# Kernel optimization log

Hardware: AMD Instinct MI355X
Metric: run time of the kernel (lower is better)

Reference implementation:

```python
import jax, jax.numpy as jnp
import numpy as np

N = 16384
E = 262144

def _deg_norm(idx, n):
    deg = jax.ops.segment_sum(jnp.ones((idx.shape[0],), jnp.float32), idx, num_segments=n)
    return jnp.where(deg > 0, deg ** -0.5, 0.0)  # DGL norm='both' with zero-in-degree allowed

def _graph_conv(x, W, b, edge_src, edge_dst, c_src, c_dst):
    # DGL GraphConv(norm='both'): h = D_in^{-1/2} A D_out^{-1/2} (x W) + b
    h = (x * c_src[:, None]) @ W            # [N, out] (mult-first order; linear, so equivalent)
    msg = h[edge_src]                        # gather over edges [E, out]
    agg = jax.ops.segment_sum(msg, edge_dst, num_segments=x.shape[0])
    return agg * c_dst[:, None] + b

def setup_inputs() -> dict:
    key = jax.random.key(0)
    ks = jax.random.split(key, 8)
    return {
        "features": jax.random.normal(ks[0], (N, 256), jnp.float32),
        "W1": jax.random.normal(ks[1], (256, 128), jnp.float32) * 0.05,
        "b1": jnp.zeros((128,), jnp.float32),
        "Wm": jax.random.normal(ks[2], (128, 64), jnp.float32) * 0.05,
        "bm": jnp.zeros((64,), jnp.float32),
        "Ws": jax.random.normal(ks[3], (128, 64), jnp.float32) * 0.05,
        "bs": jnp.zeros((64,), jnp.float32),
        "noise": jax.random.normal(ks[4], (N, 64), jnp.float32),
        "edge_src": jax.random.randint(ks[5], (E,), 0, N, jnp.int32),
        "edge_dst": jax.random.randint(ks[6], (E,), 0, N, jnp.int32),
    }

def reference(features, W1, b1, Wm, bm, Ws, bs, noise, edge_src, edge_dst):
    n = features.shape[0]
    c_src = _deg_norm(edge_src, n)   # out-degree norm
    c_dst = _deg_norm(edge_dst, n)   # in-degree norm
    h = jax.nn.relu(_graph_conv(features, W1, b1, edge_src, edge_dst, c_src, c_dst))
    mean = _graph_conv(h, Wm, bm, edge_src, edge_dst, c_src, c_dst)
    log_std = _graph_conv(h, Ws, bs, edge_src, edge_dst, c_src, c_dst)
    z = mean + noise * jnp.exp(log_std)      # reparameterization
    # InnerProductDecoder with act=identity (dropout inactive at eval), then sigmoid
    pre = jax.nn.sigmoid(z @ z.T)            # [N, N]
    return (pre, z)
```

## Files before the change

kernel.cpp:

```cpp
#include <hip/hip_runtime.h>
#include <hip/hip_bf16.h>


typedef short short8 __attribute__((ext_vector_type(8)));
typedef short short4v __attribute__((ext_vector_type(4)));
typedef float f32x4 __attribute__((ext_vector_type(4)));

__device__ __forceinline__ float bf2f(short s) {
  unsigned int u = ((unsigned int)(unsigned short)s) << 16;
  return __uint_as_float(u);
}

__global__ void k_deg(const int* __restrict__ src, const int* __restrict__ dst,
                      float* __restrict__ cs, float* __restrict__ cd, int E) {
  int i = blockIdx.x * blockDim.x + threadIdx.x;
  if (i < E) {
    atomicAdd(&cs[src[i]], 1.0f);
    atomicAdd(&cd[dst[i]], 1.0f);
  }
}

__global__ void __launch_bounds__(256) k_scan(const float* __restrict__ cnt,
                                              int* __restrict__ off, int n) {
  __shared__ int sums[256];
  const int t = threadIdx.x;
  const int per = n / 256;
  const int base = t * per;
  int s = 0;
  for (int i = 0; i < per; ++i) s += (int)cnt[base + i];
  sums[t] = s;
  __syncthreads();
  for (int d = 1; d < 256; d <<= 1) {
    int v = (t >= d) ? sums[t - d] : 0;
    __syncthreads();
    sums[t] += v;
    __syncthreads();
  }
  int run = t ? sums[t - 1] : 0;
  for (int i = 0; i < per; ++i) { off[base + i] = run; run += (int)cnt[base + i]; }
  if (t == 255) off[n] = run;
}

__global__ void k_cnorm(float* __restrict__ cs, float* __restrict__ cd, int n) {
  int i = blockIdx.x * blockDim.x + threadIdx.x;
  if (i < n) {
    float a = cs[i]; cs[i] = (a > 0.f) ? rsqrtf(a) : 0.f;
    float b = cd[i]; cd[i] = (b > 0.f) ? rsqrtf(b) : 0.f;
  }
}

__global__ void k_fill(const int* __restrict__ src, const int* __restrict__ dst,
                       const int* __restrict__ off, int* __restrict__ cursor,
                       int* __restrict__ elist, int E) {
  int e = blockIdx.x * blockDim.x + threadIdx.x;
  if (e < E) {
    int d = dst[e];
    int pos = atomicAdd(&cursor[d], 1);
    elist[off[d] + pos] = src[e];
  }
}

__global__ void k_wprep1(const float* __restrict__ W, short* __restrict__ hi,
                         short* __restrict__ lo) {
  int idx = blockIdx.x * 256 + threadIdx.x;
  int c = idx >> 8, k = idx & 255;
  float v = W[k * 128 + c];
  __hip_bfloat16 hb = __float2bfloat16(v);
  float hf = __bfloat162float(hb);
  __hip_bfloat16 lb = __float2bfloat16(v - hf);
  hi[c * 256 + k] = *reinterpret_cast<short*>(&hb);
  lo[c * 256 + k] = *reinterpret_cast<short*>(&lb);
}

__global__ void k_wprep2(const float* __restrict__ Wm, const float* __restrict__ Ws,
                         short* __restrict__ hi, short* __restrict__ lo) {
  int idx = blockIdx.x * 256 + threadIdx.x;
  int c = idx >> 7, k = idx & 127;
  float v = (c < 64) ? Wm[k * 64 + c] : Ws[k * 64 + (c - 64)];
  __hip_bfloat16 hb = __float2bfloat16(v);
  float hf = __bfloat162float(hb);
  __hip_bfloat16 lb = __float2bfloat16(v - hf);
  hi[c * 128 + k] = *reinterpret_cast<short*>(&hb);
  lo[c * 128 + k] = *reinterpret_cast<short*>(&lb);
}

__global__ void __launch_bounds__(256) k_enc1(const float* __restrict__ x,
                                              const short* __restrict__ wt_hi,
                                              const short* __restrict__ wt_lo,
                                              const float* __restrict__ cs,
                                              __hip_bfloat16* __restrict__ out) {
  const int wave = threadIdx.x >> 6, lane = threadIdx.x & 63;
  const int lrow = lane & 15, kq = lane >> 4;
  const int brow = blockIdx.x * 64;
  const int bcol = wave * 32;

  f32x4 acc[4][2];
#pragma unroll
  for (int i = 0; i < 4; ++i)
#pragma unroll
    for (int j = 0; j < 2; ++j) acc[i][j] = (f32x4){0.f, 0.f, 0.f, 0.f};

  float crow[4];
#pragma unroll
  for (int i = 0; i < 4; ++i) crow[i] = cs[brow + i * 16 + lrow];

  for (int ks = 0; ks < 8; ++ks) {
    short8 ahi[4], alo[4];
#pragma unroll
    for (int i = 0; i < 4; ++i) {
      const float* ap = x + (size_t)(brow + i * 16 + lrow) * 256 + ks * 32 + kq * 8;
      f32x4 a0 = *reinterpret_cast<const f32x4*>(ap);
      f32x4 a1 = *reinterpret_cast<const f32x4*>(ap + 4);
      const float c = crow[i];
      float vals[8] = {a0.x, a0.y, a0.z, a0.w, a1.x, a1.y, a1.z, a1.w};
      short8 h, l;
#pragma unroll
      for (int j = 0; j < 8; ++j) {
        float v = vals[j] * c;
        __hip_bfloat16 hb = __float2bfloat16(v);
        float hf = __bfloat162float(hb);
        __hip_bfloat16 lb = __float2bfloat16(v - hf);
        h[j] = *reinterpret_cast<short*>(&hb);
        l[j] = *reinterpret_cast<short*>(&lb);
      }
      ahi[i] = h; alo[i] = l;
    }
    short8 bhi[2], blo[2];
#pragma unroll
    for (int j = 0; j < 2; ++j) {
      size_t boff = (size_t)(bcol + j * 16 + lrow) * 256 + ks * 32 + kq * 8;
      bhi[j] = *reinterpret_cast<const short8*>(wt_hi + boff);
      blo[j] = *reinterpret_cast<const short8*>(wt_lo + boff);
    }
#pragma unroll
    for (int i = 0; i < 4; ++i)
#pragma unroll
      for (int j = 0; j < 2; ++j) {
        acc[i][j] = __builtin_amdgcn_mfma_f32_16x16x32_bf16(ahi[i], bhi[j], acc[i][j], 0, 0, 0);
        acc[i][j] = __builtin_amdgcn_mfma_f32_16x16x32_bf16(ahi[i], blo[j], acc[i][j], 0, 0, 0);
        acc[i][j] = __builtin_amdgcn_mfma_f32_16x16x32_bf16(alo[i], bhi[j], acc[i][j], 0, 0, 0);
      }
  }
#pragma unroll
  for (int i = 0; i < 4; ++i)
#pragma unroll
    for (int r = 0; r < 4; ++r) {
      int row = brow + i * 16 + kq * 4 + r;
#pragma unroll
      for (int j = 0; j < 2; ++j)
        out[(size_t)row * 128 + bcol + j * 16 + lrow] = __float2bfloat16(acc[i][j][r]);
    }
}

__global__ void __launch_bounds__(256) k_gather1(const short* __restrict__ tmp,
                                                 const int* __restrict__ off,
                                                 const int* __restrict__ elist,
                                                 const float* __restrict__ cd,
                                                 const float* __restrict__ cs,
                                                 const float* __restrict__ b,
                                                 short* __restrict__ hs) {
  const int node = blockIdx.x * 4 + (threadIdx.x >> 6);
  const int lane = threadIdx.x & 63;
  const int half = lane >> 5;
  const int c4 = (lane & 31) << 2;
  const int e0 = off[node], e1 = off[node + 1];
  f32x4 a = {0.f, 0.f, 0.f, 0.f};
  for (int e = e0 + half; e < e1; e += 2) {
    short4v v = *reinterpret_cast<const short4v*>(tmp + (size_t)elist[e] * 128 + c4);
    a.x += bf2f(v[0]); a.y += bf2f(v[1]); a.z += bf2f(v[2]); a.w += bf2f(v[3]);
  }
  a.x += __shfl_xor(a.x, 32);
  a.y += __shfl_xor(a.y, 32);
  a.z += __shfl_xor(a.z, 32);
  a.w += __shfl_xor(a.w, 32);
  if (half == 0) {
    const float c = cd[node], s = cs[node];
    f32x4 bb = *reinterpret_cast<const f32x4*>(b + c4);
    short4v r;
    {
      __hip_bfloat16 t0 = __float2bfloat16(fmaxf(a.x * c + bb.x, 0.f) * s);
      __hip_bfloat16 t1 = __float2bfloat16(fmaxf(a.y * c + bb.y, 0.f) * s);
      __hip_bfloat16 t2 = __float2bfloat16(fmaxf(a.z * c + bb.z, 0.f) * s);
      __hip_bfloat16 t3 = __float2bfloat16(fmaxf(a.w * c + bb.w, 0.f) * s);
      r[0] = *reinterpret_cast<short*>(&t0);
      r[1] = *reinterpret_cast<short*>(&t1);
      r[2] = *reinterpret_cast<short*>(&t2);
      r[3] = *reinterpret_cast<short*>(&t3);
    }
    *reinterpret_cast<short4v*>(hs + (size_t)node * 128 + c4) = r;
  }
}

__global__ void __launch_bounds__(256) k_gather2(const short* __restrict__ hs,
                                                 const int* __restrict__ off,
                                                 const int* __restrict__ elist,
                                                 const float* __restrict__ cd,
                                                 float* __restrict__ s2c) {
  const int node = blockIdx.x * 4 + (threadIdx.x >> 6);
  const int lane = threadIdx.x & 63;
  const int half = lane >> 5;
  const int c4 = (lane & 31) << 2;
  const int e0 = off[node], e1 = off[node + 1];
  f32x4 a = {0.f, 0.f, 0.f, 0.f};
  for (int e = e0 + half; e < e1; e += 2) {
    short4v v = *reinterpret_cast<const short4v*>(hs + (size_t)elist[e] * 128 + c4);
    a.x += bf2f(v[0]); a.y += bf2f(v[1]); a.z += bf2f(v[2]); a.w += bf2f(v[3]);
  }
  a.x += __shfl_xor(a.x, 32);
  a.y += __shfl_xor(a.y, 32);
  a.z += __shfl_xor(a.z, 32);
  a.w += __shfl_xor(a.w, 32);
  if (half == 0) {
    const float c = cd[node];
    *reinterpret_cast<f32x4*>(s2c + (size_t)node * 128 + c4) = a * c;
  }
}

__global__ void __launch_bounds__(256) k_zfin2(const float* __restrict__ s2c,
                                               const short* __restrict__ wt_hi,
                                               const short* __restrict__ wt_lo,
                                               const float* __restrict__ bm,
                                               const float* __restrict__ bs,
                                               const float* __restrict__ noise,
                                               float* __restrict__ z,
                                               __hip_bfloat16* __restrict__ zb) {
  __shared__ float ys[64][128];
  const int wave = threadIdx.x >> 6, lane = threadIdx.x & 63;
  const int lrow = lane & 15, kq = lane >> 4;
  const int brow = blockIdx.x * 64;
  const int bcol = wave * 32;

  f32x4 acc[4][2];
#pragma unroll
  for (int i = 0; i < 4; ++i)
#pragma unroll
    for (int j = 0; j < 2; ++j) acc[i][j] = (f32x4){0.f, 0.f, 0.f, 0.f};

  for (int ks = 0; ks < 4; ++ks) {
    short8 ahi[4], alo[4];
#pragma unroll
    for (int i = 0; i < 4; ++i) {
      const float* ap = s2c + (size_t)(brow + i * 16 + lrow) * 128 + ks * 32 + kq * 8;
      f32x4 a0 = *reinterpret_cast<const f32x4*>(ap);
      f32x4 a1 = *reinterpret_cast<const f32x4*>(ap + 4);
      float vals[8] = {a0.x, a0.y, a0.z, a0.w, a1.x, a1.y, a1.z, a1.w};
      short8 h, l;
#pragma unroll
      for (int j = 0; j < 8; ++j) {
        float v = vals[j];
        __hip_bfloat16 hb = __float2bfloat16(v);
        float hf = __bfloat162float(hb);
        __hip_bfloat16 lb = __float2bfloat16(v - hf);
        h[j] = *reinterpret_cast<short*>(&hb);
        l[j] = *reinterpret_cast<short*>(&lb);
      }
      ahi[i] = h; alo[i] = l;
    }
    short8 bhi[2], blo[2];
#pragma unroll
    for (int j = 0; j < 2; ++j) {
      size_t boff = (size_t)(bcol + j * 16 + lrow) * 128 + ks * 32 + kq * 8;
      bhi[j] = *reinterpret_cast<const short8*>(wt_hi + boff);
      blo[j] = *reinterpret_cast<const short8*>(wt_lo + boff);
    }
#pragma unroll
    for (int i = 0; i < 4; ++i)
#pragma unroll
      for (int j = 0; j < 2; ++j) {
        acc[i][j] = __builtin_amdgcn_mfma_f32_16x16x32_bf16(ahi[i], bhi[j], acc[i][j], 0, 0, 0);
        acc[i][j] = __builtin_amdgcn_mfma_f32_16x16x32_bf16(ahi[i], blo[j], acc[i][j], 0, 0, 0);
        acc[i][j] = __builtin_amdgcn_mfma_f32_16x16x32_bf16(alo[i], bhi[j], acc[i][j], 0, 0, 0);
      }
  }
#pragma unroll
  for (int j = 0; j < 2; ++j) {
    const int col = bcol + j * 16 + lrow;
    const float bias = (col < 64) ? bm[col] : bs[col - 64];
#pragma unroll
    for (int i = 0; i < 4; ++i)
#pragma unroll
      for (int r = 0; r < 4; ++r)
        ys[i * 16 + kq * 4 + r][col] = acc[i][j][r] + bias;
  }
  __syncthreads();
  const int t = threadIdx.x;
#pragma unroll
  for (int q = 0; q < 16; ++q) {
    int idx = t + 256 * q;
    int row = idx >> 6, c = idx & 63;
    float m = ys[row][c], ls = ys[row][c + 64];
    float zv = m + noise[(size_t)(brow + row) * 64 + c] * __expf(ls);
    z[(size_t)(brow + row) * 64 + c]  = zv;
    zb[(size_t)(brow + row) * 64 + c] = __float2bfloat16(zv);
  }
}

__global__ void __launch_bounds__(256) k_zz_mfma(const short* __restrict__ zb,
                                                 float* __restrict__ pre, int n) {
  const int wave = threadIdx.x >> 6, lane = threadIdx.x & 63;
  const int wr = wave >> 1, wc = wave & 1;
  const int brow = blockIdx.y * 128 + wr * 64;
  const int bcol = blockIdx.x * 128 + wc * 64;
  const int lrow = lane & 15;
  const int kq = lane >> 4;

  short8 afrag[2][4], bfrag[2][4];
#pragma unroll
  for (int tt = 0; tt < 4; ++tt) {
#pragma unroll
    for (int ks = 0; ks < 2; ++ks) {
      afrag[ks][tt] = *reinterpret_cast<const short8*>(
          zb + (size_t)(brow + tt * 16 + lrow) * 64 + ks * 32 + kq * 8);
      bfrag[ks][tt] = *reinterpret_cast<const short8*>(
          zb + (size_t)(bcol + tt * 16 + lrow) * 64 + ks * 32 + kq * 8);
    }
  }

  f32x4 acc[4][4];
#pragma unroll
  for (int i = 0; i < 4; ++i)
#pragma unroll
    for (int j = 0; j < 4; ++j) acc[i][j] = (f32x4){0.f, 0.f, 0.f, 0.f};

#pragma unroll
  for (int i = 0; i < 4; ++i)
#pragma unroll
    for (int j = 0; j < 4; ++j) {
      acc[i][j] = __builtin_amdgcn_mfma_f32_16x16x32_bf16(afrag[0][i], bfrag[0][j], acc[i][j], 0, 0, 0);
      acc[i][j] = __builtin_amdgcn_mfma_f32_16x16x32_bf16(afrag[1][i], bfrag[1][j], acc[i][j], 0, 0, 0);
    }

  const int crow0 = kq * 4;
#pragma unroll
  for (int i = 0; i < 4; ++i) {
#pragma unroll
    for (int r = 0; r < 4; ++r) {
      size_t rowoff = (size_t)(brow + i * 16 + crow0 + r) * (size_t)n;
#pragma unroll
      for (int j = 0; j < 4; ++j) {
        float e = __expf(-acc[i][j][r]);
        pre[rowoff + bcol + j * 16 + lrow] = __builtin_amdgcn_rcpf(1.f + e);
      }
    }
  }
}

extern "C" void kernel_launch(void* const* d_in, const int* in_sizes, int n_in,
                              void* d_out, int out_size, void* d_ws, size_t ws_size,
                              hipStream_t stream) {
  const float* feat  = (const float*)d_in[0];
  const float* W1    = (const float*)d_in[1];
  const float* b1    = (const float*)d_in[2];
  const float* Wm    = (const float*)d_in[3];
  const float* bm    = (const float*)d_in[4];
  const float* Ws    = (const float*)d_in[5];
  const float* bs    = (const float*)d_in[6];
  const float* noise = (const float*)d_in[7];
  const int* esrc    = (const int*)d_in[8];
  const int* edst    = (const int*)d_in[9];

  const int N = in_sizes[0] / 256;
  const int E = in_sizes[8];

  float* out = (float*)d_out;
  float* z   = out + (size_t)N * N;

  char* ws = (char*)d_ws;
  float* c_src  = (float*)(ws + 0);
  float* c_dst  = (float*)(ws + 65536);
  int*   cursor = (int*)  (ws + 131072);
  int*   off    = (int*)  (ws + 196608);
  int*   elist  = (int*)  (ws + 327680);
  short* w1t_hi = (short*)(ws + 1376256);
  short* w1t_lo = (short*)(ws + 1441792);
  short* w2t_hi = (short*)(ws + 1507328);
  short* w2t_lo = (short*)(ws + 1540096);
  short* bufA   = (short*)(ws + 2097152);
  short* hsb    = (short*)(ws + 6291456);
  float* s2c    = (float*)(ws + 10485760);
  __hip_bfloat16* zb = (__hip_bfloat16*)(ws + 18874368);

  k_wprep1<<<128, 256, 0, stream>>>(W1, w1t_hi, w1t_lo);
  k_wprep2<<<64, 256, 0, stream>>>(Wm, Ws, w2t_hi, w2t_lo);

  hipMemsetAsync(ws, 0, 196608, stream);
  k_deg<<<(E + 255) / 256, 256, 0, stream>>>(esrc, edst, c_src, c_dst, E);
  k_scan<<<1, 256, 0, stream>>>(c_dst, off, N);
  k_cnorm<<<(N + 255) / 256, 256, 0, stream>>>(c_src, c_dst, N);
  k_fill<<<(E + 255) / 256, 256, 0, stream>>>(esrc, edst, off, cursor, elist, E);

  k_enc1<<<N / 64, 256, 0, stream>>>(feat, w1t_hi, w1t_lo, c_src, (__hip_bfloat16*)bufA);
  k_gather1<<<N / 4, 256, 0, stream>>>(bufA, off, elist, c_dst, c_src, b1, hsb);

  k_gather2<<<N / 4, 256, 0, stream>>>(hsb, off, elist, c_dst, s2c);
  k_zfin2<<<N / 64, 256, 0, stream>>>(s2c, w2t_hi, w2t_lo, bm, bs, noise, z, zb);

  dim3 zgrid(N / 128, N / 128);
  k_zz_mfma<<<zgrid, 256, 0, stream>>>((const short*)zb, out, N);
}
```

Baseline: 371.7 us.

## Merge prep kernels, widen gather loads, and use nontemporal stores for output

Merges the two weight-prep kernels into one launch and folds the degree normalization into the single-block scan kernel, so two launches disappear. Both gather kernels now have each lane load 8 bf16 values (16 bytes). Four edge groups per wave are unrolled by two to keep more loads in flight, then reduced with two shuffles. The large N×N sigmoid output is written with nontemporal stores to reduce cache pollution. The single-block scan now also handles all rsqrt normalization, which lengthens that serial step.

```diff
diff --git a/kernel.cpp b/kernel.cpp
--- a/kernel.cpp
+++ b/kernel.cpp
@@ -3,12 +3,15 @@
 
 
 typedef short short8 __attribute__((ext_vector_type(8)));
-typedef short short4v __attribute__((ext_vector_type(4)));
 typedef float f32x4 __attribute__((ext_vector_type(4)));
 
 __device__ __forceinline__ float bf2f(short s) {
   unsigned int u = ((unsigned int)(unsigned short)s) << 16;
   return __uint_as_float(u);
+}
+__device__ __forceinline__ short f2bf(float f) {
+  __hip_bfloat16 h = __float2bfloat16(f);
+  return *reinterpret_cast<short*>(&h);
 }
 
 __global__ void k_deg(const int* __restrict__ src, const int* __restrict__ dst,
@@ -20,14 +23,15 @@
   }
 }
 
-__global__ void __launch_bounds__(256) k_scan(const float* __restrict__ cnt,
+__global__ void __launch_bounds__(256) k_scan(float* __restrict__ cs,
+                                              float* __restrict__ cd,
                                               int* __restrict__ off, int n) {
   __shared__ int sums[256];
   const int t = threadIdx.x;
   const int per = n / 256;
   const int base = t * per;
   int s = 0;
-  for (int i = 0; i < per; ++i) s += (int)cnt[base + i];
+  for (int i = 0; i < per; ++i) s += (int)cd[base + i];
   sums[t] = s;
   __syncthreads();
   for (int d = 1; d < 256; d <<= 1) {
@@ -37,16 +41,14 @@
     __syncthreads();
   }
   int run = t ? sums[t - 1] : 0;
-  for (int i = 0; i < per; ++i) { off[base + i] = run; run += (int)cnt[base + i]; }
+  for (int i = 0; i < per; ++i) {
+    float cnt = cd[base + i];
+    off[base + i] = run; run += (int)cnt;
+    cd[base + i] = (cnt > 0.f) ? rsqrtf(cnt) : 0.f;
+    float a = cs[base + i];
+    cs[base + i] = (a > 0.f) ? rsqrtf(a) : 0.f;
+  }
   if (t == 255) off[n] = run;
-}
-
-__global__ void k_cnorm(float* __restrict__ cs, float* __restrict__ cd, int n) {
-  int i = blockIdx.x * blockDim.x + threadIdx.x;
-  if (i < n) {
-    float a = cs[i]; cs[i] = (a > 0.f) ? rsqrtf(a) : 0.f;
-    float b = cd[i]; cd[i] = (b > 0.f) ? rsqrtf(b) : 0.f;
-  }
 }
 
 __global__ void k_fill(const int* __restrict__ src, const int* __restrict__ dst,
@@ -60,28 +62,27 @@
   }
 }
 
-__global__ void k_wprep1(const float* __restrict__ W, short* __restrict__ hi,
-                         short* __restrict__ lo) {
-  int idx = blockIdx.x * 256 + threadIdx.x;
-  int c = idx >> 8, k = idx & 255;
-  float v = W[k * 128 + c];
-  __hip_bfloat16 hb = __float2bfloat16(v);
-  float hf = __bfloat162float(hb);
-  __hip_bfloat16 lb = __float2bfloat16(v - hf);
-  hi[c * 256 + k] = *reinterpret_cast<short*>(&hb);
-  lo[c * 256 + k] = *reinterpret_cast<short*>(&lb);
-}
-
-__global__ void k_wprep2(const float* __restrict__ Wm, const float* __restrict__ Ws,
-                         short* __restrict__ hi, short* __restrict__ lo) {
-  int idx = blockIdx.x * 256 + threadIdx.x;
-  int c = idx >> 7, k = idx & 127;
-  float v = (c < 64) ? Wm[k * 64 + c] : Ws[k * 64 + (c - 64)];
-  __hip_bfloat16 hb = __float2bfloat16(v);
-  float hf = __bfloat162float(hb);
-  __hip_bfloat16 lb = __float2bfloat16(v - hf);
-  hi[c * 128 + k] = *reinterpret_cast<short*>(&hb);
-  lo[c * 128 + k] = *reinterpret_cast<short*>(&lb);
+__global__ void k_wprep(const float* __restrict__ W1, const float* __restrict__ Wm,
+                        const float* __restrict__ Ws,
+                        short* __restrict__ w1hi, short* __restrict__ w1lo,
+                        short* __restrict__ w2hi, short* __restrict__ w2lo) {
+  if (blockIdx.x < 128) {
+    int idx = blockIdx.x * 256 + threadIdx.x;
+    int c = idx >> 8, k = idx & 255;
+    float v = W1[k * 128 + c];
+    short hb = f2bf(v);
+    float hf = bf2f(hb);
+    w1hi[c * 256 + k] = hb;
+    w1lo[c * 256 + k] = f2bf(v - hf);
+  } else {
+    int idx = (blockIdx.x - 128) * 256 + threadIdx.x;
+    int c = idx >> 7, k = idx & 127;
+    float v = (c < 64) ? Wm[k * 64 + c] : Ws[k * 64 + (c - 64)];
+    short hb = f2bf(v);
+    float hf = bf2f(hb);
+    w2hi[c * 128 + k] = hb;
+    w2lo[c * 128 + k] = f2bf(v - hf);
+  }
 }
 
 __global__ void __launch_bounds__(256) k_enc1(const float* __restrict__ x,
@@ -117,11 +118,9 @@
 #pragma unroll
       for (int j = 0; j < 8; ++j) {
         float v = vals[j] * c;
-        __hip_bfloat16 hb = __float2bfloat16(v);
-        float hf = __bfloat162float(hb);
-        __hip_bfloat16 lb = __float2bfloat16(v - hf);
-        h[j] = *reinterpret_cast<short*>(&hb);
-        l[j] = *reinterpret_cast<short*>(&lb);
+        short hb = f2bf(v);
+        h[j] = hb;
+        l[j] = f2bf(v - bf2f(hb));
       }
       ahi[i] = h; alo[i] = l;
     }
@@ -161,33 +160,43 @@
                                                  short* __restrict__ hs) {
   const int node = blockIdx.x * 4 + (threadIdx.x >> 6);
   const int lane = threadIdx.x & 63;
-  const int half = lane >> 5;
-  const int c4 = (lane & 31) << 2;
+  const int grp = lane >> 4;
+  const int c8 = (lane & 15) * 8;
   const int e0 = off[node], e1 = off[node + 1];
-  f32x4 a = {0.f, 0.f, 0.f, 0.f};
-  for (int e = e0 + half; e < e1; e += 2) {
-    short4v v = *reinterpret_cast<const short4v*>(tmp + (size_t)elist[e] * 128 + c4);
-    a.x += bf2f(v[0]); a.y += bf2f(v[1]); a.z += bf2f(v[2]); a.w += bf2f(v[3]);
-  }
-  a.x += __shfl_xor(a.x, 32);
-  a.y += __shfl_xor(a.y, 32);
-  a.z += __shfl_xor(a.z, 32);
-  a.w += __shfl_xor(a.w, 32);
-  if (half == 0) {
+  f32x4 a0 = {0.f, 0.f, 0.f, 0.f}, a1 = {0.f, 0.f, 0.f, 0.f};
+  int e = e0 + grp;
+  for (; e + 4 < e1; e += 8) {
+    short8 v0 = *reinterpret_cast<const short8*>(tmp + (size_t)elist[e] * 128 + c8);
+    short8 v1 = *reinterpret_cast<const short8*>(tmp + (size_t)elist[e + 4] * 128 + c8);
+    a0.x += bf2f(v0[0]); a0.y += bf2f(v0[1]); a0.z += bf2f(v0[2]); a0.w += bf2f(v0[3]);
+    a1.x += bf2f(v0[4]); a1.y += bf2f(v0[5]); a1.z += bf2f(v0[6]); a1.w += bf2f(v0[7]);
+    a0.x += bf2f(v1[0]); a0.y += bf2f(v1[1]); a0.z += bf2f(v1[2]); a0.w += bf2f(v1[3]);
+    a1.x += bf2f(v1[4]); a1.y += bf2f(v1[5]); a1.z += bf2f(v1[6]); a1.w += bf2f(v1[7]);
+  }
+  if (e < e1) {
+    short8 v0 = *reinterpret_cast<const short8*>(tmp + (size_t)elist[e] * 128 + c8);
+    a0.x += bf2f(v0[0]); a0.y += bf2f(v0[1]); a0.z += bf2f(v0[2]); a0.w += bf2f(v0[3]);
+    a1.x += bf2f(v0[4]); a1.y += bf2f(v0[5]); a1.z += bf2f(v0[6]); a1.w += bf2f(v0[7]);
+  }
+#pragma unroll
+  for (int k = 0; k < 4; ++k) {
+    a0[k] += __shfl_xor(a0[k], 16); a0[k] += __shfl_xor(a0[k], 32);
+    a1[k] += __shfl_xor(a1[k], 16); a1[k] += __shfl_xor(a1[k], 32);
+  }
+  if (grp == 0) {
     const float c = cd[node], s = cs[node];
-    f32x4 bb = *reinterpret_cast<const f32x4*>(b + c4);
-    short4v r;
-    {
-      __hip_bfloat16 t0 = __float2bfloat16(fmaxf(a.x * c + bb.x, 0.f) * s);
-      __hip_bfloat16 t1 = __float2bfloat16(fmaxf(a.y * c + bb.y, 0.f) * s);
-      __hip_bfloat16 t2 = __float2bfloat16(fmaxf(a.z * c + bb.z, 0.f) * s);
-      __hip_bfloat16 t3 = __float2bfloat16(fmaxf(a.w * c + bb.w, 0.f) * s);
-      r[0] = *reinterpret_cast<short*>(&t0);
-      r[1] = *reinterpret_cast<short*>(&t1);
-      r[2] = *reinterpret_cast<short*>(&t2);
-      r[3] = *reinterpret_cast<short*>(&t3);
-    }
-    *reinterpret_cast<short4v*>(hs + (size_t)node * 128 + c4) = r;
+    f32x4 b0 = *reinterpret_cast<const f32x4*>(b + c8);
+    f32x4 b1v = *reinterpret_cast<const f32x4*>(b + c8 + 4);
+    short8 r;
+    r[0] = f2bf(fmaxf(a0.x * c + b0.x, 0.f) * s);
+    r[1] = f2bf(fmaxf(a0.y * c + b0.y, 0.f) * s);
+    r[2] = f2bf(fmaxf(a0.z * c + b0.z, 0.f) * s);
+    r[3] = f2bf(fmaxf(a0.w * c + b0.w, 0.f) * s);
+    r[4] = f2bf(fmaxf(a1.x * c + b1v.x, 0.f) * s);
+    r[5] = f2bf(fmaxf(a1.y * c + b1v.y, 0.f) * s);
+    r[6] = f2bf(fmaxf(a1.z * c + b1v.z, 0.f) * s);
+    r[7] = f2bf(fmaxf(a1.w * c + b1v.w, 0.f) * s);
+    *reinterpret_cast<short8*>(hs + (size_t)node * 128 + c8) = r;
   }
 }
 
@@ -198,21 +207,34 @@
                                                  float* __restrict__ s2c) {
   const int node = blockIdx.x * 4 + (threadIdx.x >> 6);
   const int lane = threadIdx.x & 63;
-  const int half = lane >> 5;
-  const int c4 = (lane & 31) << 2;
+  const int grp = lane >> 4;
+  const int c8 = (lane & 15) * 8;
   const int e0 = off[node], e1 = off[node + 1];
-  f32x4 a = {0.f, 0.f, 0.f, 0.f};
-  for (int e = e0 + half; e < e1; e += 2) {
-    short4v v = *reinterpret_cast<const short4v*>(hs + (size_t)elist[e] * 128 + c4);
-    a.x += bf2f(v[0]); a.y += bf2f(v[1]); a.z += bf2f(v[2]); a.w += bf2f(v[3]);
-  }
-  a.x += __shfl_xor(a.x, 32);
-  a.y += __shfl_xor(a.y, 32);
-  a.z += __shfl_xor(a.z, 32);
-  a.w += __shfl_xor(a.w, 32);
-  if (half == 0) {
+  f32x4 a0 = {0.f, 0.f, 0.f, 0.f}, a1 = {0.f, 0.f, 0.f, 0.f};
+  int e = e0 + grp;
+  for (; e + 4 < e1; e += 8) {
+    short8 v0 = *reinterpret_cast<const short8*>(hs + (size_t)elist[e] * 128 + c8);
+    short8 v1 = *reinterpret_cast<const short8*>(hs + (size_t)elist[e + 4] * 128 + c8);
+    a0.x += bf2f(v0[0]); a0.y += bf2f(v0[1]); a0.z += bf2f(v0[2]); a0.w += bf2f(v0[3]);
+    a1.x += bf2f(v0[4]); a1.y += bf2f(v0[5]); a1.z += bf2f(v0[6]); a1.w += bf2f(v0[7]);
+    a0.x += bf2f(v1[0]); a0.y += bf2f(v1[1]); a0.z += bf2f(v1[2]); a0.w += bf2f(v1[3]);
+    a1.x += bf2f(v1[4]); a1.y += bf2f(v1[5]); a1.z += bf2f(v1[6]); a1.w += bf2f(v1[7]);
+  }
+  if (e < e1) {
+    short8 v0 = *reinterpret_cast<const short8*>(hs + (size_t)elist[e] * 128 + c8);
+    a0.x += bf2f(v0[0]); a0.y += bf2f(v0[1]); a0.z += bf2f(v0[2]); a0.w += bf2f(v0[3]);
+    a1.x += bf2f(v0[4]); a1.y += bf2f(v0[5]); a1.z += bf2f(v0[6]); a1.w += bf2f(v0[7]);
+  }
+#pragma unroll
+  for (int k = 0; k < 4; ++k) {
+    a0[k] += __shfl_xor(a0[k], 16); a0[k] += __shfl_xor(a0[k], 32);
+    a1[k] += __shfl_xor(a1[k], 16); a1[k] += __shfl_xor(a1[k], 32);
+  }
+  if (grp == 0) {
     const float c = cd[node];
-    *reinterpret_cast<f32x4*>(s2c + (size_t)node * 128 + c4) = a * c;
+    float* p = s2c + (size_t)node * 128 + c8;
+    *reinterpret_cast<f32x4*>(p)     = a0 * c;
+    *reinterpret_cast<f32x4*>(p + 4) = a1 * c;
   }
 }
 
@@ -248,11 +270,9 @@
 #pragma unroll
       for (int j = 0; j < 8; ++j) {
         float v = vals[j];
-        __hip_bfloat16 hb = __float2bfloat16(v);
-        float hf = __bfloat162float(hb);
-        __hip_bfloat16 lb = __float2bfloat16(v - hf);
-        h[j] = *reinterpret_cast<short*>(&hb);
-        l[j] = *reinterpret_cast<short*>(&lb);
+        short hb = f2bf(v);
+        h[j] = hb;
+        l[j] = f2bf(v - bf2f(hb));
       }
       ahi[i] = h; alo[i] = l;
     }
@@ -339,7 +359,8 @@
 #pragma unroll
       for (int j = 0; j < 4; ++j) {
         float e = __expf(-acc[i][j][r]);
-        pre[rowoff + bcol + j * 16 + lrow] = __builtin_amdgcn_rcpf(1.f + e);
+        __builtin_nontemporal_store(__builtin_amdgcn_rcpf(1.f + e),
+                                    &pre[rowoff + bcol + j * 16 + lrow]);
       }
     }
   }
@@ -380,13 +401,11 @@
   float* s2c    = (float*)(ws + 10485760);
   __hip_bfloat16* zb = (__hip_bfloat16*)(ws + 18874368);
 
-  k_wprep1<<<128, 256, 0, stream>>>(W1, w1t_hi, w1t_lo);
-  k_wprep2<<<64, 256, 0, stream>>>(Wm, Ws, w2t_hi, w2t_lo);
+  k_wprep<<<192, 256, 0, stream>>>(W1, Wm, Ws, w1t_hi, w1t_lo, w2t_hi, w2t_lo);
 
   hipMemsetAsync(ws, 0, 196608, stream);
   k_deg<<<(E + 255) / 256, 256, 0, stream>>>(esrc, edst, c_src, c_dst, E);
-  k_scan<<<1, 256, 0, stream>>>(c_dst, off, N);
-  k_cnorm<<<(N + 255) / 256, 256, 0, stream>>>(c_src, c_dst, N);
+  k_scan<<<1, 256, 0, stream>>>(c_src, c_dst, off, N);
   k_fill<<<(E + 255) / 256, 256, 0, stream>>>(esrc, edst, off, cursor, elist, E);
 
   k_enc1<<<N / 64, 256, 0, stream>>>(feat, w1t_hi, w1t_lo, c_src, (__hip_bfloat16*)bufA);
```

Measured after the change: 427.0 us. +14.9%, slower.
